# Kernel optimization log

Measured on AMD Instinct MI355X. Metric: run time of the kernel, lower is better.

## Reference

```python
import jax, jax.numpy as jnp
import numpy as np

N = 256      # max_num_nodes (padded nodes per graph)
H = 8        # attention heads
F = 128      # feature_dim
L = 9        # n_layers
INFLA = 6.0  # MCL inflation
EPS = 1e-6


def _layernorm(x, g, b):
    mu = x.mean(-1, keepdims=True)
    var = ((x - mu) ** 2).mean(-1, keepdims=True)
    return (x - mu) / jnp.sqrt(var + 1e-5) * g + b


def _get_mcl(adj):
    # Markov-cluster style power iteration with inflation every 3rd step (num=6)
    m = adj / (adj.sum(-1, keepdims=True) + EPS)
    r = m
    for i in range(6):
        r = m @ r
        if (i + 1) % 3 == 0:
            r = r ** INFLA
        r = r / (r.sum(-1, keepdims=True) + EPS)
    return r


def _forward(input_x, edge_attr, gcn_lin_w, gcn_root_emb, gcn_edge_w,
             gcn_norm_g, gcn_norm_b, ln_in_g, ln_in_b, ln_ffn_g, ln_ffn_b,
             mcl_w, q_w, k_w, v_w, merge_w, merge_b,
             ffn_w1, ffn_b1, ffn_w2, ffn_b2, final_g, final_b,
             edge_index, n_counts, root):
    BN = input_x.shape[0]
    B = BN // N
    dh = F // H
    row, col = edge_index[0], edge_index[1]

    # --- adjacency / padding masks (built once, as in GC_T.forward) ---
    valid = jnp.arange(N)[None, :] < n_counts[:, None]                    # [B,N]
    eb, es, et = row // N, row % N, col % N
    adj = jnp.zeros((B, N, N), bool).at[eb, es, et].set(True)
    adj = adj | (jnp.eye(N, dtype=bool)[None] & valid[:, :, None])        # self loops on valid nodes
    pad = ~(valid[:, :, None] & valid[:, None, :])
    pad_bias = jnp.where(pad, -1024.0, 0.0)[..., None]                    # [B,N,N,1] (broadcast over H)
    mcl = _get_mcl(adj.astype(input_x.dtype))[..., None]                  # [B,N,N,1]

    # --- GCN degree normalization (degree of row index, +1) ---
    deg = jnp.zeros((BN,), input_x.dtype).at[row].add(1.0) + 1.0
    dis = deg ** -0.5
    enorm = (dis[row] * dis[col])[:, None]                                # [E,1]

    out = input_x.reshape(B, N, F)
    for i in range(L):
        # ---- GCNConv: gather-relu-scatter message passing ----
        res = out
        h = out.reshape(BN, F) @ gcn_lin_w[i].T                           # [BN,F]
        ee = edge_attr @ gcn_edge_w[i].T                                  # [E,F]
        msg = enorm * jax.nn.relu(h[row] + ee)                            # x_j = x[row]
        agg = jax.ops.segment_sum(msg, col, num_segments=BN)              # aggregate at target
        g = agg + jax.nn.relu(h + gcn_root_emb[i][root]) / deg[:, None]
        g = jax.nn.relu(_layernorm(g, gcn_norm_g[i], gcn_norm_b[i]))
        out = g.reshape(B, N, F) + res

        # ---- Encoder: biased multi-head attention + FFN ----
        bias4 = (pad_bias + mcl * mcl_w[i][:, 0]).transpose(0, 3, 1, 2)   # [B,H,N,N]
        x = out
        q = (x @ q_w[i].T).reshape(B, N, H, dh).transpose(0, 2, 1, 3) * (dh ** -0.5)
        k = (x @ k_w[i].T).reshape(B, N, H, dh).transpose(0, 2, 1, 3)
        v = (x @ v_w[i].T).reshape(B, N, H, dh).transpose(0, 2, 1, 3)
        att = jax.nn.softmax(jnp.einsum('bhnd,bhmd->bhnm', q, k) + bias4, axis=-1)
        o = jnp.einsum('bhnm,bhmd->bhnd', att, v).transpose(0, 2, 1, 3).reshape(B, N, F)
        o = o @ merge_w[i].T + merge_b[i]
        x = _layernorm(o + x, ln_in_g[i], ln_in_b[i])
        f = jax.nn.gelu(x @ ffn_w1[i].T + ffn_b1[i], approximate=False)
        f = f @ ffn_w2[i].T + ffn_b2[i]
        out = _layernorm(x + f, ln_ffn_g[i], ln_ffn_b[i])

    return _layernorm(out, final_g, final_b)


def setup_inputs() -> dict:
    key = jax.random.key(0)
    ks = jax.random.split(key, 16)
    B, E = 16, 65536
    s = 0.02 * L ** -0.5
    w = lambda k, shape: jax.random.normal(k, shape, jnp.float32) * s
    return {
        'input_x': jax.random.normal(ks[0], (B * N, F), jnp.float32),
        'edge_attr': jax.random.normal(ks[1], (E, 7), jnp.float32),
        'gcn_lin_w': w(ks[2], (L, F, F)),
        'gcn_root_emb': jax.random.normal(ks[3], (L, 2, F), jnp.float32) * 0.02,
        'gcn_edge_w': w(ks[4], (L, F, 7)),
        'gcn_norm_g': jnp.ones((L, F), jnp.float32),
        'gcn_norm_b': jnp.zeros((L, F), jnp.float32),
        'ln_in_g': jnp.ones((L, F), jnp.float32),
        'ln_in_b': jnp.zeros((L, F), jnp.float32),
        'ln_ffn_g': jnp.ones((L, F), jnp.float32),
        'ln_ffn_b': jnp.zeros((L, F), jnp.float32),
        'mcl_w': w(ks[5], (L, H, 1)),
        'q_w': w(ks[6], (L, F, F)),
        'k_w': w(ks[7], (L, F, F)),
        'v_w': w(ks[8], (L, F, F)),
        'merge_w': w(ks[9], (L, F, F)),
        'merge_b': jnp.zeros((L, F), jnp.float32),
        'ffn_w1': w(ks[10], (L, 2 * F, F)),
        'ffn_b1': jnp.zeros((L, 2 * F), jnp.float32),
        'ffn_w2': w(ks[11], (L, F, 2 * F)),
        'ffn_b2': jnp.zeros((L, F), jnp.float32),
        'final_g': jnp.ones((F,), jnp.float32),
        'final_b': jnp.zeros((F,), jnp.float32),
        'edge_index': jax.random.randint(ks[12], (2, E), 0, B * N),
        'n_counts': jax.random.randint(ks[13], (B,), 1, N + 1),
        'root': jax.random.randint(ks[14], (B * N,), 0, 2),
    }


def reference(input_x, edge_attr, gcn_lin_w, gcn_root_emb, gcn_edge_w,
              gcn_norm_g, gcn_norm_b, ln_in_g, ln_in_b, ln_ffn_g, ln_ffn_b,
              mcl_w, q_w, k_w, v_w, merge_w, merge_b,
              ffn_w1, ffn_b1, ffn_w2, ffn_b2, final_g, final_b,
              edge_index, n_counts, root):
    return _forward(input_x, edge_attr, gcn_lin_w, gcn_root_emb, gcn_edge_w,
                    gcn_norm_g, gcn_norm_b, ln_in_g, ln_in_b, ln_ffn_g, ln_ffn_b,
                    mcl_w, q_w, k_w, v_w, merge_w, merge_b,
                    ffn_w1, ffn_b1, ffn_w2, ffn_b2, final_g, final_b,
                    edge_index, n_counts, root)
```

## Files before the change

### kernel.cpp

```cpp
#include <hip/hip_runtime.h>
#include <hip/hip_bf16.h>
#include <math.h>

#define NLAYER 9

typedef unsigned short u16;
typedef __attribute__((ext_vector_type(8))) short short8;
typedef __attribute__((ext_vector_type(4))) float f32x4;

__device__ inline u16 f2bf(float x) {
  unsigned int u = __float_as_uint(x);
  unsigned int r = (u + 0x7fffu + ((u >> 16) & 1u)) >> 16;
  return (u16)r;
}
__device__ inline float bf2f(u16 s) { return __uint_as_float(((unsigned int)s) << 16); }
__device__ inline float gelu_exact(float x) {
  return 0.5f * x * (1.0f + erff(x * 0.7071067811865476f));
}

#define BF16_ONE 0x3F80u

__global__ void setup1_kernel(const int* __restrict__ ei, u16* __restrict__ adjb,
                              float* __restrict__ deg, int* __restrict__ ccount, int E, int EB,
                              const float* __restrict__ s0, const float* __restrict__ s1,
                              const float* __restrict__ s2, const float* __restrict__ s3,
                              const float* __restrict__ s4, const float* __restrict__ s5,
                              const float* __restrict__ s6, u16* __restrict__ d0,
                              u16* __restrict__ d1, u16* __restrict__ d2,
                              u16* __restrict__ d3, u16* __restrict__ d4,
                              u16* __restrict__ d5, u16* __restrict__ d6) {
  int bid = blockIdx.x;
  if (bid < EB) {
    int e = bid * 256 + threadIdx.x;
    if (e >= E) return;
    int r = ei[e], c = ei[E + e];
    int b = r >> 8;
    adjb[((size_t)b << 16) + ((size_t)(r & 255) << 8) + (c & 255)] = (u16)BF16_ONE;
    atomicAdd(&deg[r], 1.0f);
    atomicAdd(&ccount[c], 1);
  } else {
    int idx = bid - EB;
    int f = idx / 72, cb = idx % 72;
    const float* s;
    u16* d;
    int n;
    switch (f) {
      case 0: s = s0; d = d0; n = NLAYER * 4096; break;
      case 1: s = s1; d = d1; n = NLAYER * 4096; break;
      case 2: s = s2; d = d2; n = NLAYER * 4096; break;
      case 3: s = s3; d = d3; n = NLAYER * 4096; break;
      case 4: s = s4; d = d4; n = NLAYER * 4096; break;
      case 5: s = s5; d = d5; n = NLAYER * 8192; break;
      default: s = s6; d = d6; n = NLAYER * 8192; break;
    }
    for (int i = cb * 256 + threadIdx.x; i < n; i += 72 * 256) {
      float4 v = ((const float4*)s)[i];
      u16 p4[4] = {f2bf(v.x), f2bf(v.y), f2bf(v.z), f2bf(v.w)};
      ((ushort4*)d)[i] = *(ushort4*)p4;
    }
  }
}

__global__ __launch_bounds__(1024) void setup2_kernel(
    const int* __restrict__ nc, u16* __restrict__ adjb, float* __restrict__ deg,
    float* __restrict__ dis, const int* __restrict__ ccount, int* __restrict__ rowptr, int BN,
    const float* __restrict__ x, const u16* __restrict__ wlin0, float* __restrict__ outb,
    float* __restrict__ hbuf) {
  __shared__ u16 smem_u[64 * 136];
  int bid = blockIdx.x;
  int t = threadIdx.x;
  int NSL = BN >> 10;
  if (bid < NSL) {
    int n = bid * 1024 + t;
    int b = n >> 8, i = n & 255;
    if (i < nc[b]) adjb[((size_t)b << 16) + ((size_t)i << 8) + i] = (u16)BF16_ONE;
    float d = deg[n] + 1.0f;
    deg[n] = d;
    dis[n] = rsqrtf(d);
  } else if (bid == NSL) {
    int* part = (int*)smem_u;
    int base = t * 4;
    int c[4], s = 0;
#pragma unroll
    for (int i = 0; i < 4; i++) { c[i] = (base + i < BN) ? ccount[base + i] : 0; s += c[i]; }
    part[t] = s;
    __syncthreads();
    for (int o = 1; o < 1024; o <<= 1) {
      int v = (t >= o) ? part[t - o] : 0;
      __syncthreads();
      part[t] += v;
      __syncthreads();
    }
    int excl = part[t] - s;
#pragma unroll
    for (int i = 0; i < 4; i++) {
      if (base + i < BN) rowptr[base + i] = excl;
      excl += c[i];
    }
    if (t == 1023) rowptr[BN] = part[1023];
  } else {
    int m0 = (bid - NSL - 1) * 64;
    for (int i = t; i < 8192; i += 1024) {
      int row = i >> 7, col = i & 127;
      float v = x[(size_t)(m0 + row) * 128 + col];
      outb[(size_t)(m0 + row) * 128 + col] = v;
      smem_u[row * 136 + col] = f2bf(v);
    }
    __syncthreads();
    int w = t >> 6, lane = t & 63;
    int m16 = lane & 15, quad = lane >> 4;
    int rowg = w >> 2, colg = w & 3;
    int c0 = colg * 32;
    f32x4 acc[2] = {{0.f, 0.f, 0.f, 0.f}, {0.f, 0.f, 0.f, 0.f}};
#pragma unroll
    for (int k0 = 0; k0 < 128; k0 += 32) {
      short8 a = *(const short8*)(smem_u + (rowg * 16 + m16) * 136 + k0 + quad * 8);
#pragma unroll
      for (int tt = 0; tt < 2; tt++) {
        short8 bb =
            *(const short8*)(wlin0 + (size_t)(c0 + tt * 16 + m16) * 128 + k0 + quad * 8);
        acc[tt] = __builtin_amdgcn_mfma_f32_16x16x32_bf16(a, bb, acc[tt], 0, 0, 0);
      }
    }
#pragma unroll
    for (int tt = 0; tt < 2; tt++)
#pragma unroll
      for (int reg = 0; reg < 4; reg++)
        hbuf[(size_t)(m0 + rowg * 16 + quad * 4 + reg) * 128 + c0 + tt * 16 + m16] =
            acc[tt][reg];
  }
}

__global__ __launch_bounds__(256) void setup3_kernel(const u16* __restrict__ adjb,
                                                     float* __restrict__ rsinv,
                                                     const int* __restrict__ ei,
                                                     const float* __restrict__ dis,
                                                     const int* __restrict__ rowptr,
                                                     int* __restrict__ fill,
                                                     int* __restrict__ src_s,
                                                     int* __restrict__ eidx_s,
                                                     float* __restrict__ enorm_s, int E,
                                                     int BN) {
  int bid = blockIdx.x;
  int w = threadIdx.x >> 6, lane = threadIdx.x & 63;
  if (bid < (BN >> 2)) {
    int row = bid * 4 + w;
    ushort4 v4 = *(const ushort4*)(adjb + (size_t)row * 256 + lane * 4);
    float s = bf2f(v4.x) + bf2f(v4.y) + bf2f(v4.z) + bf2f(v4.w);
#pragma unroll
    for (int o = 32; o > 0; o >>= 1) s += __shfl_xor(s, o, 64);
    if (lane == 0) rsinv[row] = 1.f / (s + 1e-6f);
  } else {
    int e = (bid - (BN >> 2)) * 256 + threadIdx.x;
    if (e >= E) return;
    int r = ei[e], c = ei[E + e];
    int pos = rowptr[c] + atomicAdd(&fill[c], 1);
    src_s[pos] = r;
    eidx_s[pos] = e;
    enorm_s[pos] = dis[r] * dis[c];
  }
}

__global__ __launch_bounds__(256) void mcl_prep_kernel(u16* __restrict__ mb,
                                                       const float* __restrict__ rsinv,
                                                       u16* __restrict__ rT) {
  int b = blockIdx.z;
  u16* MB = mb + ((size_t)b << 16);
  u16* RT = rT + ((size_t)b << 16);
  int r0 = blockIdx.x * 64, c0 = blockIdx.y * 64;
  __shared__ float ts[64][65];
  int t = threadIdx.x;
  int i = t >> 2, jb = (t & 3) * 16;
  float riv = rsinv[(b << 8) + r0 + i];
#pragma unroll
  for (int g = 0; g < 4; g++) {
    int j = jb + g * 4;
    ushort4 u4 = *(const ushort4*)(MB + (size_t)(r0 + i) * 256 + c0 + j);
    float vx = bf2f(u4.x) * riv, vy = bf2f(u4.y) * riv, vz = bf2f(u4.z) * riv,
          vw = bf2f(u4.w) * riv;
    ts[i][j] = vx; ts[i][j + 1] = vy; ts[i][j + 2] = vz; ts[i][j + 3] = vw;
    u16 p4[4] = {f2bf(vx), f2bf(vy), f2bf(vz), f2bf(vw)};
    *(ushort4*)(MB + (size_t)(r0 + i) * 256 + c0 + j) = *(ushort4*)p4;
  }
  __syncthreads();
#pragma unroll
  for (int g = 0; g < 4; g++) {
    int j = jb + g * 4;
    u16 p4[4] = {f2bf(ts[j][i]), f2bf(ts[j + 1][i]), f2bf(ts[j + 2][i]), f2bf(ts[j + 3][i])};
    *(ushort4*)(RT + (size_t)(c0 + i) * 256 + r0 + j) = *(ushort4*)p4;
  }
}

__global__ __launch_bounds__(256) void mcl_iter_kernel(const u16* __restrict__ rT,
                                                       const u16* __restrict__ mb,
                                                       u16* __restrict__ rTn,
                                                       float* __restrict__ mclr,
                                                       int inflate, int fin) {
  __shared__ float red[64];
  int b = blockIdx.x >> 4, i0 = (blockIdx.x & 15) * 16;
  int w = threadIdx.x >> 6, lane = threadIdx.x & 63;
  int m16 = lane & 15, quad = lane >> 4;
  const u16* A = rT + ((size_t)b << 16);
  const u16* Bm = mb + ((size_t)b << 16);
  f32x4 acc[4];
#pragma unroll
  for (int tj = 0; tj < 4; tj++) acc[tj] = (f32x4){0.f, 0.f, 0.f, 0.f};
  for (int k0 = 0; k0 < 256; k0 += 32) {
    short8 bb = *(const short8*)(Bm + (size_t)(i0 + m16) * 256 + k0 + quad * 8);
#pragma unroll
    for (int tj = 0; tj < 4; tj++) {
      short8 a = *(const short8*)(A + (size_t)(w * 64 + tj * 16 + m16) * 256 + k0 + quad * 8);
      acc[tj] = __builtin_amdgcn_mfma_f32_16x16x32_bf16(a, bb, acc[tj], 0, 0, 0);
    }
  }
  float ps = 0.f;
#pragma unroll
  for (int tj = 0; tj < 4; tj++)
#pragma unroll
    for (int reg = 0; reg < 4; reg++) {
      float v = acc[tj][reg];
      if (inflate) { float v2 = v * v; v = v2 * v2 * v2; }
      acc[tj][reg] = v;
      ps += v;
    }
  ps += __shfl_xor(ps, 16, 64);
  ps += __shfl_xor(ps, 32, 64);
  if (quad == 0) red[w * 16 + m16] = ps;
  __syncthreads();
  float tot = red[m16] + red[16 + m16] + red[32 + m16] + red[48 + m16];
  float inv = 1.f / (tot + 1e-6f);
  if (fin) {
    float* dst = mclr + ((size_t)b << 16);
#pragma unroll
    for (int tj = 0; tj < 4; tj++)
#pragma unroll
      for (int reg = 0; reg < 4; reg++) {
        int j = w * 64 + tj * 16 + quad * 4 + reg;
        dst[(size_t)(i0 + m16) * 256 + j] = acc[tj][reg] * inv;
      }
  } else {
    u16* dst = rTn + ((size_t)b << 16);
#pragma unroll
    for (int tj = 0; tj < 4; tj++)
#pragma unroll
      for (int reg = 0; reg < 4; reg++) {
        int j = w * 64 + tj * 16 + quad * 4 + reg;
        dst[(size_t)j * 256 + i0 + m16] = f2bf(acc[tj][reg] * inv);
      }
  }
}

__global__ __launch_bounds__(256) void gcn_ln_kernel(
    const int* __restrict__ rowptr, const int* __restrict__ src_s,
    const int* __restrict__ eidx_s, const float* __restrict__ enorm_s,
    const float* __restrict__ ea, const float* __restrict__ We, const float* __restrict__ h,
    const float* __restrict__ remb, const int* __restrict__ root,
    const float* __restrict__ deg, const float* __restrict__ gamma,
    const float* __restrict__ beta, float* __restrict__ out, u16* __restrict__ out16) {
  __shared__ float Wt[7 * 128];
  __shared__ float part[2][2][128];
  for (int idx = threadIdx.x; idx < 896; idx += 256) {
    int f = idx & 127, k = idx >> 7;
    Wt[k * 128 + f] = We[f * 7 + k];
  }
  __syncthreads();
  int w = threadIdx.x >> 6, lane = threadIdx.x & 63;
  int nodeSlot = w >> 1, wv = w & 1;
  int n = blockIdx.x * 2 + nodeSlot;
  int f0 = lane, f1 = lane + 64;
  int p0 = rowptr[n], p1 = rowptr[n + 1];
  float a0 = 0.f, a1 = 0.f;
  int p = p0 + wv;
  int r = 0, e = 0;
  float en = 0.f, h0 = 0.f, h1 = 0.f;
  if (p < p1) {
    r = src_s[p];
    e = eidx_s[p];
    en = enorm_s[p];
    h0 = h[(size_t)r * 128 + f0];
    h1 = h[(size_t)r * 128 + f1];
  }
  for (; p < p1; p += 2) {
    int enx = 0;
    float ennx = 0.f, hn0 = 0.f, hn1 = 0.f;
    if (p + 2 < p1) {
      int rn = src_s[p + 2];
      enx = eidx_s[p + 2];
      ennx = enorm_s[p + 2];
      hn0 = h[(size_t)rn * 128 + f0];
      hn1 = h[(size_t)rn * 128 + f1];
    }
    const float* eae = ea + (size_t)e * 7;
    float d0 = 0.f, d1 = 0.f;
#pragma unroll
    for (int k = 0; k < 7; k++) {
      float ev = eae[k];
      d0 += ev * Wt[k * 128 + f0];
      d1 += ev * Wt[k * 128 + f1];
    }
    a0 += en * fmaxf(h0 + d0, 0.f);
    a1 += en * fmaxf(h1 + d1, 0.f);
    e = enx;
    en = ennx;
    h0 = hn0;
    h1 = hn1;
  }
  part[nodeSlot][wv][lane] = a0;
  part[nodeSlot][wv][64 + lane] = a1;
  __syncthreads();
  if (wv == 0) {
    a0 = part[nodeSlot][0][lane] + part[nodeSlot][1][lane];
    a1 = part[nodeSlot][0][64 + lane] + part[nodeSlot][1][64 + lane];
    float invd = 1.0f / deg[n];
    const float* re = remb + root[n] * 128;
    size_t base = (size_t)n * 128;
    float g0 = a0 + fmaxf(h[base + f0] + re[f0], 0.f) * invd;
    float g1 = a1 + fmaxf(h[base + f1] + re[f1], 0.f) * invd;
    float s = g0 + g1, ss = g0 * g0 + g1 * g1;
#pragma unroll
    for (int o = 32; o > 0; o >>= 1) {
      s += __shfl_xor(s, o, 64);
      ss += __shfl_xor(ss, o, 64);
    }
    float mu = s * 0.0078125f;
    float var = ss * 0.0078125f - mu * mu;
    float rs = rsqrtf(var + 1e-5f);
    float y0 = fmaxf((g0 - mu) * rs * gamma[f0] + beta[f0], 0.f) + out[base + f0];
    float y1 = fmaxf((g1 - mu) * rs * gamma[f1] + beta[f1], 0.f) + out[base + f1];
    out[base + f0] = y0;
    out[base + f1] = y1;
    out16[base + f0] = f2bf(y0);
    out16[base + f1] = f2bf(y1);
  }
}

__global__ __launch_bounds__(256) void attn_qkv_kernel(
    const u16* __restrict__ x16, const u16* __restrict__ wq, const u16* __restrict__ wk,
    const u16* __restrict__ wv, const float* __restrict__ mclr,
    const float* __restrict__ mclw, const int* __restrict__ ncnt, u16* __restrict__ o) {
  __shared__ float ks[256][16];
  __shared__ float vs[256][16];
  __shared__ float qs[64][16];
  int qt = blockIdx.x, hh = blockIdx.y, b = blockIdx.z;
  int t = threadIdx.x;
  int w = t >> 6, lane = t & 63;
  int m16 = lane & 15, quad = lane >> 4;
  const u16* bk = wk + (size_t)(hh * 16 + m16) * 128 + quad * 8;
  const u16* bv = wv + (size_t)(hh * 16 + m16) * 128 + quad * 8;
#pragma unroll
  for (int tj = 0; tj < 4; tj++) {
    int rb = w * 64 + tj * 16;
    const u16* arow = x16 + (size_t)(b * 256 + rb + m16) * 128 + quad * 8;
    f32x4 ak = {0.f, 0.f, 0.f, 0.f}, av = {0.f, 0.f, 0.f, 0.f};
#pragma unroll
    for (int k0 = 0; k0 < 128; k0 += 32) {
      short8 a = *(const short8*)(arow + k0);
      ak = __builtin_amdgcn_mfma_f32_16x16x32_bf16(a, *(const short8*)(bk + k0), ak, 0, 0, 0);
      av = __builtin_amdgcn_mfma_f32_16x16x32_bf16(a, *(const short8*)(bv + k0), av, 0, 0, 0);
    }
#pragma unroll
    for (int reg = 0; reg < 4; reg++) {
      ks[rb + quad * 4 + reg][m16] = ak[reg];
      vs[rb + quad * 4 + reg][m16] = av[reg];
    }
  }
  {
    const u16* bq = wq + (size_t)(hh * 16 + m16) * 128 + quad * 8;
    const u16* arow = x16 + (size_t)(b * 256 + qt * 64 + w * 16 + m16) * 128 + quad * 8;
    f32x4 aq = {0.f, 0.f, 0.f, 0.f};
#pragma unroll
    for (int k0 = 0; k0 < 128; k0 += 32) {
      short8 a = *(const short8*)(arow + k0);
      aq = __builtin_amdgcn_mfma_f32_16x16x32_bf16(a, *(const short8*)(bq + k0), aq, 0, 0, 0);
    }
#pragma unroll
    for (int reg = 0; reg < 4; reg++) qs[w * 16 + quad * 4 + reg][m16] = aq[reg] * 0.25f;
  }
  __syncthreads();
  int i = qt * 64 + (t >> 2);
  int d0 = (t & 3) * 4;
  int nc = ncnt[b];
  bool vi = i < nc;
  int jpad = vi ? nc : 257;
  float wh = mclw[hh];
  float qv[4] = {qs[t >> 2][d0], qs[t >> 2][d0 + 1], qs[t >> 2][d0 + 2], qs[t >> 2][d0 + 3]};
  const float* mrow = mclr + ((size_t)(b * 256 + i)) * 256;
  float acc[4] = {0.f, 0.f, 0.f, 0.f};
  float lsum = 0.f;
  for (int j0 = 0; j0 < 256; j0 += 8) {
    float4 mc0 = *(const float4*)(mrow + j0);
    float4 mc1 = *(const float4*)(mrow + j0 + 4);
    float mcv[8] = {mc0.x, mc0.y, mc0.z, mc0.w, mc1.x, mc1.y, mc1.z, mc1.w};
#pragma unroll
    for (int jj = 0; jj < 8; jj++) {
      int j = j0 + jj;
      float s = qv[0] * ks[j][d0] + qv[1] * ks[j][d0 + 1] + qv[2] * ks[j][d0 + 2] +
                qv[3] * ks[j][d0 + 3];
      s += __shfl_xor(s, 1, 64);
      s += __shfl_xor(s, 2, 64);
      float bias = mcv[jj] * wh + ((j >= jpad) ? -1024.f : 0.f);
      float pe = __expf(s + bias);
      lsum += pe;
      acc[0] += pe * vs[j][d0];
      acc[1] += pe * vs[j][d0 + 1];
      acc[2] += pe * vs[j][d0 + 2];
      acc[3] += pe * vs[j][d0 + 3];
    }
  }
  float inv = 1.f / lsum;
  u16 p4[4] = {f2bf(acc[0] * inv), f2bf(acc[1] * inv), f2bf(acc[2] * inv), f2bf(acc[3] * inv)};
  *(ushort4*)(o + ((size_t)(b * 256 + i) * 128 + hh * 16 + d0)) = *(ushort4*)p4;
}

__global__ __launch_bounds__(256) void merge_ffn_kernel(
    const u16* __restrict__ ob16, const u16* __restrict__ Wm, const float* __restrict__ mb,
    const float* __restrict__ gam1, const float* __restrict__ bet1,
    const u16* __restrict__ W1, const float* __restrict__ b1, const u16* __restrict__ W2,
    const float* __restrict__ b2, const float* __restrict__ gam2,
    const float* __restrict__ bet2, float* __restrict__ outb,
    const u16* __restrict__ wlin_next, float* __restrict__ hbuf,
    const float* __restrict__ fing, const float* __restrict__ finb) {
  __shared__ float redS[64], redSS[64];
  __shared__ u16 st[16 * 136];
  __shared__ u16 f1s[16 * 264];
  int tid = threadIdx.x;
  int w = tid >> 6, lane = tid & 63;
  int m16 = lane & 15, quad = lane >> 4;
  int m0 = blockIdx.x * 16;
  f32x4 acc[2] = {{0.f, 0.f, 0.f, 0.f}, {0.f, 0.f, 0.f, 0.f}};
  {
    const u16* arow = ob16 + (size_t)(m0 + m16) * 128 + quad * 8;
#pragma unroll
    for (int k0 = 0; k0 < 128; k0 += 32) {
      short8 a = *(const short8*)(arow + k0);
#pragma unroll
      for (int t = 0; t < 2; t++) {
        short8 bb = *(const short8*)(Wm + (size_t)(w * 32 + t * 16 + m16) * 128 + k0 + quad * 8);
        acc[t] = __builtin_amdgcn_mfma_f32_16x16x32_bf16(a, bb, acc[t], 0, 0, 0);
      }
    }
  }
  float s4[4] = {0.f, 0.f, 0.f, 0.f}, ss4[4] = {0.f, 0.f, 0.f, 0.f};
#pragma unroll
  for (int t = 0; t < 2; t++) {
    int col = w * 32 + t * 16 + m16;
    float bi = mb[col];
#pragma unroll
    for (int reg = 0; reg < 4; reg++) {
      int row = m0 + quad * 4 + reg;
      float v = acc[t][reg] + bi + outb[(size_t)row * 128 + col];
      acc[t][reg] = v;
      s4[reg] += v;
      ss4[reg] += v * v;
    }
  }
#pragma unroll
  for (int o = 1; o <= 8; o <<= 1)
#pragma unroll
    for (int reg = 0; reg < 4; reg++) {
      s4[reg] += __shfl_xor(s4[reg], o, 64);
      ss4[reg] += __shfl_xor(ss4[reg], o, 64);
    }
  if (m16 == 0) {
#pragma unroll
    for (int reg = 0; reg < 4; reg++) {
      redS[w * 16 + quad * 4 + reg] = s4[reg];
      redSS[w * 16 + quad * 4 + reg] = ss4[reg];
    }
  }
  __syncthreads();
  float mu[4], rsd[4];
#pragma unroll
  for (int reg = 0; reg < 4; reg++) {
    int r = quad * 4 + reg;
    float S = redS[r] + redS[16 + r] + redS[32 + r] + redS[48 + r];
    float SS = redSS[r] + redSS[16 + r] + redSS[32 + r] + redSS[48 + r];
    mu[reg] = S * 0.0078125f;
    float var = SS * 0.0078125f - mu[reg] * mu[reg];
    rsd[reg] = rsqrtf(var + 1e-5f);
  }
  float xr[2][4];
#pragma unroll
  for (int t = 0; t < 2; t++) {
    int col = w * 32 + t * 16 + m16;
    float g = gam1[col], be = bet1[col];
#pragma unroll
    for (int reg = 0; reg < 4; reg++) {
      float y = (acc[t][reg] - mu[reg]) * rsd[reg] * g + be;
      xr[t][reg] = y;
      st[(quad * 4 + reg) * 136 + col] = f2bf(y);
    }
  }
  __syncthreads();
  {
    f32x4 acc1[4];
#pragma unroll
    for (int t = 0; t < 4; t++) acc1[t] = (f32x4){0.f, 0.f, 0.f, 0.f};
#pragma unroll
    for (int k0 = 0; k0 < 128; k0 += 32) {
      short8 a = *(const short8*)(st + m16 * 136 + k0 + quad * 8);
#pragma unroll
      for (int t = 0; t < 4; t++) {
        short8 bb = *(const short8*)(W1 + (size_t)(w * 64 + t * 16 + m16) * 128 + k0 + quad * 8);
        acc1[t] = __builtin_amdgcn_mfma_f32_16x16x32_bf16(a, bb, acc1[t], 0, 0, 0);
      }
    }
#pragma unroll
    for (int t = 0; t < 4; t++) {
      int col = w * 64 + t * 16 + m16;
      float bi = b1[col];
#pragma unroll
      for (int reg = 0; reg < 4; reg++)
        f1s[(quad * 4 + reg) * 264 + col] = f2bf(gelu_exact(acc1[t][reg] + bi));
    }
  }
  __syncthreads();
#pragma unroll
  for (int t = 0; t < 2; t++) acc[t] = (f32x4){0.f, 0.f, 0.f, 0.f};
#pragma unroll
  for (int k0 = 0; k0 < 256; k0 += 32) {
    short8 a = *(const short8*)(f1s + m16 * 264 + k0 + quad * 8);
#pragma unroll
    for (int t = 0; t < 2; t++) {
      short8 bb = *(const short8*)(W2 + (size_t)(w * 32 + t * 16 + m16) * 256 + k0 + quad * 8);
      acc[t] = __builtin_amdgcn_mfma_f32_16x16x32_bf16(a, bb, acc[t], 0, 0, 0);
    }
  }
#pragma unroll
  for (int reg = 0; reg < 4; reg++) { s4[reg] = 0.f; ss4[reg] = 0.f; }
#pragma unroll
  for (int t = 0; t < 2; t++) {
    int col = w * 32 + t * 16 + m16;
    float bi = b2[col];
#pragma unroll
    for (int reg = 0; reg < 4; reg++) {
      float v = acc[t][reg] + bi + xr[t][reg];
      acc[t][reg] = v;
      s4[reg] += v;
      ss4[reg] += v * v;
    }
  }
#pragma unroll
  for (int o = 1; o <= 8; o <<= 1)
#pragma unroll
    for (int reg = 0; reg < 4; reg++) {
      s4[reg] += __shfl_xor(s4[reg], o, 64);
      ss4[reg] += __shfl_xor(ss4[reg], o, 64);
    }
  __syncthreads();
  if (m16 == 0) {
#pragma unroll
    for (int reg = 0; reg < 4; reg++) {
      redS[w * 16 + quad * 4 + reg] = s4[reg];
      redSS[w * 16 + quad * 4 + reg] = ss4[reg];
    }
  }
  __syncthreads();
#pragma unroll
  for (int reg = 0; reg < 4; reg++) {
    int r = quad * 4 + reg;
    float S = redS[r] + redS[16 + r] + redS[32 + r] + redS[48 + r];
    float SS = redSS[r] + redSS[16 + r] + redSS[32 + r] + redSS[48 + r];
    mu[reg] = S * 0.0078125f;
    float var = SS * 0.0078125f - mu[reg] * mu[reg];
    rsd[reg] = rsqrtf(var + 1e-5f);
  }
#pragma unroll
  for (int t = 0; t < 2; t++) {
    int col = w * 32 + t * 16 + m16;
    float g = gam2[col], be = bet2[col];
#pragma unroll
    for (int reg = 0; reg < 4; reg++)
      acc[t][reg] = (acc[t][reg] - mu[reg]) * rsd[reg] * g + be;
  }
  if (fing) {
    float s2[4] = {0.f, 0.f, 0.f, 0.f}, ss2[4] = {0.f, 0.f, 0.f, 0.f};
#pragma unroll
    for (int t = 0; t < 2; t++)
#pragma unroll
      for (int reg = 0; reg < 4; reg++) {
        float v = acc[t][reg];
        s2[reg] += v;
        ss2[reg] += v * v;
      }
#pragma unroll
    for (int o = 1; o <= 8; o <<= 1)
#pragma unroll
      for (int reg = 0; reg < 4; reg++) {
        s2[reg] += __shfl_xor(s2[reg], o, 64);
        ss2[reg] += __shfl_xor(ss2[reg], o, 64);
      }
    __syncthreads();
    if (m16 == 0) {
#pragma unroll
      for (int reg = 0; reg < 4; reg++) {
        redS[w * 16 + quad * 4 + reg] = s2[reg];
        redSS[w * 16 + quad * 4 + reg] = ss2[reg];
      }
    }
    __syncthreads();
#pragma unroll
    for (int reg = 0; reg < 4; reg++) {
      int r = quad * 4 + reg;
      float S = redS[r] + redS[16 + r] + redS[32 + r] + redS[48 + r];
      float SS = redSS[r] + redSS[16 + r] + redSS[32 + r] + redSS[48 + r];
      mu[reg] = S * 0.0078125f;
      float var = SS * 0.0078125f - mu[reg] * mu[reg];
      rsd[reg] = rsqrtf(var + 1e-5f);
    }
#pragma unroll
    for (int t = 0; t < 2; t++) {
      int col = w * 32 + t * 16 + m16;
      float g = fing[col], be = finb[col];
#pragma unroll
      for (int reg = 0; reg < 4; reg++) {
        int row = m0 + quad * 4 + reg;
        outb[(size_t)row * 128 + col] = (acc[t][reg] - mu[reg]) * rsd[reg] * g + be;
      }
    }
    return;
  }
#pragma unroll
  for (int t = 0; t < 2; t++) {
    int col = w * 32 + t * 16 + m16;
#pragma unroll
    for (int reg = 0; reg < 4; reg++) {
      int row = m0 + quad * 4 + reg;
      float y = acc[t][reg];
      outb[(size_t)row * 128 + col] = y;
      st[(quad * 4 + reg) * 136 + col] = f2bf(y);
    }
  }
  __syncthreads();
  {
    f32x4 acc2[2] = {{0.f, 0.f, 0.f, 0.f}, {0.f, 0.f, 0.f, 0.f}};
#pragma unroll
    for (int k0 = 0; k0 < 128; k0 += 32) {
      short8 a = *(const short8*)(st + m16 * 136 + k0 + quad * 8);
#pragma unroll
      for (int t = 0; t < 2; t++) {
        short8 bb =
            *(const short8*)(wlin_next + (size_t)(w * 32 + t * 16 + m16) * 128 + k0 + quad * 8);
        acc2[t] = __builtin_amdgcn_mfma_f32_16x16x32_bf16(a, bb, acc2[t], 0, 0, 0);
      }
    }
#pragma unroll
    for (int t = 0; t < 2; t++)
#pragma unroll
      for (int reg = 0; reg < 4; reg++)
        hbuf[(size_t)(m0 + quad * 4 + reg) * 128 + w * 32 + t * 16 + m16] = acc2[t][reg];
  }
}

extern "C" void kernel_launch(void* const* d_in, const int* in_sizes, int n_in,
                              void* d_out, int out_size, void* d_ws, size_t ws_size,
                              hipStream_t stream) {
  const float* input_x = (const float*)d_in[0];
  const float* edge_attr = (const float*)d_in[1];
  const float* gcn_lin_w = (const float*)d_in[2];
  const float* gcn_root = (const float*)d_in[3];
  const float* gcn_edge_w = (const float*)d_in[4];
  const float* gcn_ng = (const float*)d_in[5];
  const float* gcn_nb = (const float*)d_in[6];
  const float* ln_in_g = (const float*)d_in[7];
  const float* ln_in_b = (const float*)d_in[8];
  const float* ln_ffn_g = (const float*)d_in[9];
  const float* ln_ffn_b = (const float*)d_in[10];
  const float* mcl_w = (const float*)d_in[11];
  const float* q_w = (const float*)d_in[12];
  const float* k_w = (const float*)d_in[13];
  const float* v_w = (const float*)d_in[14];
  const float* merge_w = (const float*)d_in[15];
  const float* merge_b = (const float*)d_in[16];
  const float* ffn_w1 = (const float*)d_in[17];
  const float* ffn_b1 = (const float*)d_in[18];
  const float* ffn_w2 = (const float*)d_in[19];
  const float* ffn_b2 = (const float*)d_in[20];
  const float* final_g = (const float*)d_in[21];
  const float* final_b = (const float*)d_in[22];
  const int* edge_index = (const int*)d_in[23];
  const int* n_counts = (const int*)d_in[24];
  const int* root = (const int*)d_in[25];

  const int E = in_sizes[23] / 2;
  const int B = in_sizes[24];
  const int BN = B * 256;
  const int EB = (E + 255) / 256;

  float* ws = (float*)d_ws;
  size_t off = 0;
  auto alloc = [&](size_t n) {
    off = (off + 3) & ~(size_t)3;
    float* q = ws + off;
    off += n;
    return q;
  };
  const size_t NN2 = (size_t)B * 256 * 256;
  const size_t XF = (size_t)BN * 128;
  float* mclr = alloc(NN2);
  float* hbuf = alloc(XF);
  float* deg = alloc(BN);
  int* ccount = (int*)alloc(BN);
  int* fill = (int*)alloc(BN);
  float* dis = alloc(BN);
  float* rsinv = alloc(BN);
  int* rowptr = (int*)alloc(BN + 1);
  int* src_s = (int*)alloc(E);
  int* eidx_s = (int*)alloc(E);
  float* enorm_s = alloc(E);
  u16* mb16 = (u16*)alloc(NN2 / 2);
  u16* rT16 = (u16*)alloc(NN2 / 2);
  u16* cT16 = (u16*)alloc(NN2 / 2);
  u16* ob16 = (u16*)alloc(XF / 2);
  u16* outb16 = (u16*)alloc(XF / 2);
  u16* wlin16 = (u16*)alloc((size_t)NLAYER * 8192);
  u16* wq16 = (u16*)alloc((size_t)NLAYER * 8192);
  u16* wk16 = (u16*)alloc((size_t)NLAYER * 8192);
  u16* wv16 = (u16*)alloc((size_t)NLAYER * 8192);
  u16* wm16 = (u16*)alloc((size_t)NLAYER * 8192);
  u16* wf116 = (u16*)alloc((size_t)NLAYER * 16384);
  u16* wf216 = (u16*)alloc((size_t)NLAYER * 16384);
  float* outb = (float*)d_out;

  hipMemsetAsync(mb16, 0, NN2 * sizeof(u16), stream);
  hipMemsetAsync(deg, 0, 3 * BN * sizeof(float), stream);
  setup1_kernel<<<EB + 504, 256, 0, stream>>>(edge_index, mb16, deg, ccount, E, EB, gcn_lin_w,
                                              q_w, k_w, v_w, merge_w, ffn_w1, ffn_w2, wlin16,
                                              wq16, wk16, wv16, wm16, wf116, wf216);
  setup2_kernel<<<(BN >> 10) + 1 + (BN >> 6), 1024, 0, stream>>>(
      n_counts, mb16, deg, dis, ccount, rowptr, BN, input_x, wlin16, outb, hbuf);
  setup3_kernel<<<BN / 4 + EB, 256, 0, stream>>>(mb16, rsinv, edge_index, dis, rowptr, fill,
                                                 src_s, eidx_s, enorm_s, E, BN);
  dim3 mmg(4, 4, B);
  mcl_prep_kernel<<<mmg, 256, 0, stream>>>(mb16, rsinv, rT16);
  {
    u16 *cur = rT16, *nxt = cT16;
    for (int it = 0; it < 6; it++) {
      int inflate = (it == 2 || it == 5) ? 1 : 0;
      mcl_iter_kernel<<<16 * B, 256, 0, stream>>>(cur, mb16, nxt, mclr, inflate,
                                                  it == 5 ? 1 : 0);
      u16* tmp = cur;
      cur = nxt;
      nxt = tmp;
    }
  }

  dim3 ag(4, 8, B);
  for (int l = 0; l < NLAYER; l++) {
    gcn_ln_kernel<<<BN / 2, 256, 0, stream>>>(
        rowptr, src_s, eidx_s, enorm_s, edge_attr, gcn_edge_w + (size_t)l * 896, hbuf,
        gcn_root + (size_t)l * 256, root, deg, gcn_ng + l * 128, gcn_nb + l * 128, outb,
        outb16);
    attn_qkv_kernel<<<ag, 256, 0, stream>>>(outb16, wq16 + (size_t)l * 16384,
                                            wk16 + (size_t)l * 16384,
                                            wv16 + (size_t)l * 16384, mclr, mcl_w + l * 8,
                                            n_counts, ob16);
    const u16* wnext = (l + 1 < NLAYER) ? (wlin16 + (size_t)(l + 1) * 16384) : wlin16;
    const float* fg = (l == NLAYER - 1) ? final_g : nullptr;
    const float* fb = (l == NLAYER - 1) ? final_b : nullptr;
    merge_ffn_kernel<<<BN / 16, 256, 0, stream>>>(
        ob16, wm16 + (size_t)l * 16384, merge_b + l * 128, ln_in_g + l * 128,
        ln_in_b + l * 128, wf116 + (size_t)l * 32768, ffn_b1 + l * 256,
        wf216 + (size_t)l * 32768, ffn_b2 + l * 128, ln_ffn_g + l * 128, ln_ffn_b + l * 128,
        outb, wnext, hbuf, fg, fb);
  }
}
```

Measured before the change: 764.8 us.

## Precompute squared Markov matrix to cut MCL power iterations from six to four

Adds a kernel that computes M² once and stores it both transposed and row-major. The MCL sequence then runs as M²·R with inflation, M·R, and M²·R with inflation and finalisation, which takes four matmul launches instead of six. The memsets for the adjacency and degree buffers are merged into one by reordering the workspace allocations so they are contiguous. The trade-off is an extra 256×256 buffer per graph, and the bf16 rounding now happens on M² rather than after each step, which may slightly change numerics.

```diff
diff --git a/kernel.cpp b/kernel.cpp
--- a/kernel.cpp
+++ b/kernel.cpp
@@ -191,6 +191,43 @@
   }
 }
 
+__global__ __launch_bounds__(256) void mcl_sq_kernel(const u16* __restrict__ rT,
+                                                     const u16* __restrict__ mb,
+                                                     u16* __restrict__ m2T,
+                                                     u16* __restrict__ m2rm) {
+  int b = blockIdx.x >> 4, i0 = (blockIdx.x & 15) * 16;
+  int w = threadIdx.x >> 6, lane = threadIdx.x & 63;
+  int m16 = lane & 15, quad = lane >> 4;
+  const u16* A = rT + ((size_t)b << 16);
+  const u16* Bm = mb + ((size_t)b << 16);
+  f32x4 acc[4];
+#pragma unroll
+  for (int tj = 0; tj < 4; tj++) acc[tj] = (f32x4){0.f, 0.f, 0.f, 0.f};
+  for (int k0 = 0; k0 < 256; k0 += 32) {
+    short8 bb = *(const short8*)(Bm + (size_t)(i0 + m16) * 256 + k0 + quad * 8);
+#pragma unroll
+    for (int tj = 0; tj < 4; tj++) {
+      short8 a = *(const short8*)(A + (size_t)(w * 64 + tj * 16 + m16) * 256 + k0 + quad * 8);
+      acc[tj] = __builtin_amdgcn_mfma_f32_16x16x32_bf16(a, bb, acc[tj], 0, 0, 0);
+    }
+  }
+  u16* dT = m2T + ((size_t)b << 16);
+  u16* dR = m2rm + ((size_t)b << 16);
+  int i = i0 + m16;
+#pragma unroll
+  for (int tj = 0; tj < 4; tj++) {
+    u16 pk[4];
+#pragma unroll
+    for (int reg = 0; reg < 4; reg++) {
+      int j = w * 64 + tj * 16 + quad * 4 + reg;
+      u16 v = f2bf(acc[tj][reg]);
+      dT[(size_t)j * 256 + i] = v;
+      pk[reg] = v;
+    }
+    *(ushort4*)(dR + (size_t)i * 256 + w * 64 + tj * 16 + quad * 4) = *(ushort4*)pk;
+  }
+}
+
 __global__ __launch_bounds__(256) void mcl_iter_kernel(const u16* __restrict__ rT,
                                                        const u16* __restrict__ mb,
                                                        u16* __restrict__ rTn,
@@ -697,20 +734,21 @@
   };
   const size_t NN2 = (size_t)B * 256 * 256;
   const size_t XF = (size_t)BN * 128;
-  float* mclr = alloc(NN2);
-  float* hbuf = alloc(XF);
+  u16* mb16 = (u16*)alloc(NN2 / 2);
   float* deg = alloc(BN);
   int* ccount = (int*)alloc(BN);
   int* fill = (int*)alloc(BN);
+  float* mclr = alloc(NN2);
+  float* hbuf = alloc(XF);
   float* dis = alloc(BN);
   float* rsinv = alloc(BN);
   int* rowptr = (int*)alloc(BN + 1);
   int* src_s = (int*)alloc(E);
   int* eidx_s = (int*)alloc(E);
   float* enorm_s = alloc(E);
-  u16* mb16 = (u16*)alloc(NN2 / 2);
   u16* rT16 = (u16*)alloc(NN2 / 2);
   u16* cT16 = (u16*)alloc(NN2 / 2);
+  u16* m2rm = (u16*)alloc(NN2 / 2);
   u16* ob16 = (u16*)alloc(XF / 2);
   u16* outb16 = (u16*)alloc(XF / 2);
   u16* wlin16 = (u16*)alloc((size_t)NLAYER * 8192);
@@ -722,8 +760,7 @@
   u16* wf216 = (u16*)alloc((size_t)NLAYER * 16384);
   float* outb = (float*)d_out;
 
-  hipMemsetAsync(mb16, 0, NN2 * sizeof(u16), stream);
-  hipMemsetAsync(deg, 0, 3 * BN * sizeof(float), stream);
+  hipMemsetAsync(mb16, 0, NN2 * sizeof(u16) + 3 * BN * sizeof(float), stream);
   setup1_kernel<<<EB + 504, 256, 0, stream>>>(edge_index, mb16, deg, ccount, E, EB, gcn_lin_w,
                                               q_w, k_w, v_w, merge_w, ffn_w1, ffn_w2, wlin16,
                                               wq16, wk16, wv16, wm16, wf116, wf216);
@@ -733,17 +770,10 @@
                                                  src_s, eidx_s, enorm_s, E, BN);
   dim3 mmg(4, 4, B);
   mcl_prep_kernel<<<mmg, 256, 0, stream>>>(mb16, rsinv, rT16);
-  {
-    u16 *cur = rT16, *nxt = cT16;
-    for (int it = 0; it < 6; it++) {
-      int inflate = (it == 2 || it == 5) ? 1 : 0;
-      mcl_iter_kernel<<<16 * B, 256, 0, stream>>>(cur, mb16, nxt, mclr, inflate,
-                                                  it == 5 ? 1 : 0);
-      u16* tmp = cur;
-      cur = nxt;
-      nxt = tmp;
-    }
-  }
+  mcl_sq_kernel<<<16 * B, 256, 0, stream>>>(rT16, mb16, cT16, m2rm);
+  mcl_iter_kernel<<<16 * B, 256, 0, stream>>>(cT16, m2rm, rT16, mclr, 1, 0);
+  mcl_iter_kernel<<<16 * B, 256, 0, stream>>>(rT16, mb16, cT16, mclr, 0, 0);
+  mcl_iter_kernel<<<16 * B, 256, 0, stream>>>(cT16, m2rm, rT16, mclr, 1, 1);
 
   dim3 ag(4, 8, B);
   for (int l = 0; l < NLAYER; l++) {
```

After: 744.4 us. 1.03x faster.
